# Performance work log

Measured on AMD Instinct MI355X. Metric: run time of the kernel, lower is better.

## Reference

```python
import jax, jax.numpy as jnp
import numpy as np

N, E, F_IN, HID, G = 20000, 320000, 128, 128, 64
H, D = 8, 32  # TransformerConv heads, per-head dim


def setup_inputs() -> dict:
    key = jax.random.key(0)
    ks = jax.random.split(key, 24)
    def w(k, i, o):
        return (jax.random.normal(k, (i, o), jnp.float32) / np.float32(np.sqrt(i)))
    def b(k, o):
        return jax.random.normal(k, (o,), jnp.float32) * 0.01
    inp = {
        'x': jax.random.normal(ks[0], (N, F_IN), jnp.float32),
        'edge_index': jax.random.randint(ks[1], (2, E), 0, N, jnp.int32),
        'batch': jnp.sort(jax.random.randint(ks[2], (N,), 0, G, jnp.int32)),
        # SAGEConv 1: 128 -> 128 (lin_l has bias, lin_r none)
        's1_wl': w(ks[3], 128, 128), 's1_bl': b(ks[4], 128), 's1_wr': w(ks[5], 128, 128),
        # SAGEConv 2: 128 -> 256
        's2_wl': w(ks[6], 128, 256), 's2_bl': b(ks[7], 256), 's2_wr': w(ks[8], 128, 256),
        # TransformerConv 1: 256 -> 8*32
        't1_wq': w(ks[9], 256, 256), 't1_bq': b(ks[10], 256),
        't1_wk': w(ks[11], 256, 256), 't1_bk': b(ks[12], 256),
        't1_wv': w(ks[13], 256, 256), 't1_bv': b(ks[14], 256),
        't1_ws': w(ks[15], 256, 256), 't1_bs': b(ks[16], 256),
        # TransformerConv 2
        't2_wq': w(ks[17], 256, 256), 't2_bq': b(ks[18], 256),
        't2_wk': w(ks[19], 256, 256), 't2_bk': b(ks[20], 256),
        't2_wv': w(ks[21], 256, 256), 't2_bv': b(ks[22], 256),
        't2_ws': w(ks[23], 256, 256), 't2_bs': b(jax.random.fold_in(key, 100), 256),
        # proj MLP: 256 -> 512 -> HID
        'p1_w': w(jax.random.fold_in(key, 101), 256, 512), 'p1_b': b(jax.random.fold_in(key, 102), 512),
        'p2_w': w(jax.random.fold_in(key, 103), 512, HID), 'p2_b': b(jax.random.fold_in(key, 104), HID),
    }
    return inp


def _sage(x, src, dst, wl, bl, wr):
    # PyG SAGEConv (aggr='mean'): lin_l(mean_j x_j) + lin_r(x_i)
    s = jax.ops.segment_sum(x[src], dst, num_segments=N)           # [N,F]
    cnt = jax.ops.segment_sum(jnp.ones((src.shape[0], 1), x.dtype), dst, num_segments=N)
    mean = s / jnp.maximum(cnt, 1.0)
    return mean @ wl + bl + x @ wr


def _tconv(x, src, dst, wq, bq, wk, bk, wv, bv, ws, bs):
    # PyG TransformerConv(256, 32, heads=8): per-edge attention + skip
    q = (x @ wq + bq).reshape(N, H, D)
    k = (x @ wk + bk).reshape(N, H, D)
    v = (x @ wv + bv).reshape(N, H, D)
    logits = jnp.einsum('ehd,ehd->eh', q[dst], k[src]) / np.float32(np.sqrt(D))  # [E,H]
    m = jax.ops.segment_max(logits, dst, num_segments=N)           # [N,H]
    p = jnp.exp(logits - m[dst])
    denom = jax.ops.segment_sum(p, dst, num_segments=N)
    p = p / denom[dst]                                              # softmax per target node per head
    agg = jax.ops.segment_sum(p[:, :, None] * v[src], dst, num_segments=N)  # [N,H,D]
    return agg.reshape(N, H * D) + x @ ws + bs


def reference(x, edge_index, batch, s1_wl, s1_bl, s1_wr, s2_wl, s2_bl, s2_wr,
              t1_wq, t1_bq, t1_wk, t1_bk, t1_wv, t1_bv, t1_ws, t1_bs,
              t2_wq, t2_bq, t2_wk, t2_bk, t2_wv, t2_bv, t2_ws, t2_bs,
              p1_w, p1_b, p2_w, p2_b):
    src, dst = edge_index[0], edge_index[1]
    h = jax.nn.relu(_sage(x, src, dst, s1_wl, s1_bl, s1_wr))
    h = jax.nn.relu(_sage(h, src, dst, s2_wl, s2_bl, s2_wr))
    h = jax.nn.relu(_tconv(h, src, dst, t1_wq, t1_bq, t1_wk, t1_bk, t1_wv, t1_bv, t1_ws, t1_bs))
    h = jax.nn.relu(_tconv(h, src, dst, t2_wq, t2_bq, t2_wk, t2_bk, t2_wv, t2_bv, t2_ws, t2_bs))
    # proj: ReLU -> Linear(256,512) -> ReLU -> Linear(512,HID) -> Sigmoid
    h = jax.nn.relu(h)
    h = jax.nn.relu(h @ p1_w + p1_b)
    h = jax.nn.sigmoid(h @ p2_w + p2_b)
    return jax.ops.segment_max(h, batch, num_segments=G)            # global_max_pool [G,HID]
```

## Files before the change

### kernel.cpp

```cpp
#include <hip/hip_runtime.h>
#include <hip/hip_bf16.h>
#include <math.h>

#define NN 20000
#define EE 320000
#define GG 64
#define CH 16

typedef __hip_bfloat16 bf16;
typedef __attribute__((ext_vector_type(8))) short short8;
typedef __attribute__((ext_vector_type(4))) float f32x4;
typedef unsigned int uint;
typedef unsigned short ushort;

__device__ __forceinline__ float bfr2f(ushort u) {
    union { uint i; float f; } c; c.i = ((uint)u) << 16; return c.f;
}
__device__ __forceinline__ ushort f2bfr(float f) {
    bf16 h = __float2bfloat16(f);
    return *(ushort*)&h;
}

__device__ __forceinline__ void load_lds16(const void* g, void* l) {
    __builtin_amdgcn_global_load_lds(
        (const __attribute__((address_space(1))) unsigned int*)g,
        (__attribute__((address_space(3))) unsigned int*)l, 16, 0, 0);
}

template <int KW, int NW, int KTOT, int KOFF>
__device__ __forceinline__ void tpose(int local, const float* __restrict__ W,
                                      bf16* __restrict__ Wt) {
    constexpr int SH = (KW == 128) ? 7 : ((KW == 256) ? 8 : 9);
    int n = local >> SH;
    int k = local & (KW - 1);
    Wt[(size_t)n * KTOT + KOFF + k] = __float2bfloat16(W[(size_t)k * NW + n]);
}

#define PREP_CONV  10000
#define PREP_PACK  (PREP_CONV + 3200)
#define PREP_BIAS  (PREP_PACK + 8)
#define PREP_COUNT (PREP_BIAS + 1250)

__global__ __launch_bounds__(256) void prep_kernel(
    const float* x, bf16* xm1,
    const float* s1_wr, const float* s1_wl, const float* s2_wr, const float* s2_wl,
    const float* t1_wq, const float* t1_wk, const float* t1_wv, const float* t1_ws,
    const float* t2_wq, const float* t2_wk, const float* t2_wv, const float* t2_ws,
    const float* p1_w, const float* p2_w,
    bf16* w1cat, bf16* w2cat, bf16* qw1, bf16* qw2, bf16* p1t, bf16* p2t,
    const float* b1q, const float* b1k, const float* b1v, const float* b1s,
    const float* b2q, const float* b2k, const float* b2v, const float* b2s,
    float* qb1, float* qb2,
    const int* dst, int* cnt) {
    int bid = blockIdx.x;
    int tid = threadIdx.x;
    if (bid < PREP_CONV) {
        int i = bid * 256 + tid;
        int r = i >> 7, c = i & 127;
        xm1[(size_t)r * 256 + c] = __float2bfloat16(x[i]);
    } else if (bid < PREP_PACK) {
        int i = (bid - PREP_CONV) * 256 + tid;
        if (i < 16384)        tpose<128, 128, 256, 0>(i, s1_wr, w1cat);
        else if (i < 32768)   tpose<128, 128, 256, 128>(i - 16384, s1_wl, w1cat);
        else if (i < 65536)   tpose<128, 256, 256, 0>(i - 32768, s2_wr, w2cat);
        else if (i < 98304)   tpose<128, 256, 256, 128>(i - 65536, s2_wl, w2cat);
        else if (i < 163840)  tpose<256, 256, 256, 0>(i - 98304,  t1_wq, qw1);
        else if (i < 229376)  tpose<256, 256, 256, 0>(i - 163840, t1_wk, qw1 + 65536);
        else if (i < 294912)  tpose<256, 256, 256, 0>(i - 229376, t1_wv, qw1 + 131072);
        else if (i < 360448)  tpose<256, 256, 256, 0>(i - 294912, t1_ws, qw1 + 196608);
        else if (i < 425984)  tpose<256, 256, 256, 0>(i - 360448, t2_wq, qw2);
        else if (i < 491520)  tpose<256, 256, 256, 0>(i - 425984, t2_wk, qw2 + 65536);
        else if (i < 557056)  tpose<256, 256, 256, 0>(i - 491520, t2_wv, qw2 + 131072);
        else if (i < 622592)  tpose<256, 256, 256, 0>(i - 557056, t2_ws, qw2 + 196608);
        else if (i < 753664)  tpose<256, 512, 256, 0>(i - 622592, p1_w, p1t);
        else if (i < 819200)  tpose<512, 128, 512, 0>(i - 753664, p2_w, p2t);
    } else if (bid < PREP_BIAS) {
        int i = (bid - PREP_PACK) * 256 + tid;
        if (i < 2048) {
            float* d = (i < 1024) ? qb1 : qb2;
            int j = i & 1023;
            const float* s;
            if (i < 1024) s = (j < 256) ? b1q : (j < 512) ? b1k : (j < 768) ? b1v : b1s;
            else          s = (j < 256) ? b2q : (j < 512) ? b2k : (j < 768) ? b2v : b2s;
            d[j] = s[j & 255];
        }
    } else {
        int e = (bid - PREP_BIAS) * 256 + tid;
        if (e < EE) atomicAdd(&cnt[dst[e]], 1);
    }
}

__global__ __launch_bounds__(1024) void scan_kernel(int* __restrict__ cnt,
                                                    int* __restrict__ off, int n) {
    __shared__ int wsum[16];
    __shared__ int carry_s;
    int tid = threadIdx.x;
    int lane = tid & 63, wid = tid >> 6;
    if (tid == 0) { carry_s = 0; off[0] = 0; }
    __syncthreads();
    for (int base = 0; base < n; base += 1024) {
        int idx = base + tid;
        int val = (idx < n) ? cnt[idx] : 0;
        int x = val;
        #pragma unroll
        for (int s = 1; s < 64; s <<= 1) {
            int y = __shfl_up(x, s, 64);
            if (lane >= s) x += y;
        }
        if (lane == 63) wsum[wid] = x;
        __syncthreads();
        if (tid == 0) {
            int c = carry_s;
            #pragma unroll
            for (int w = 0; w < 16; w++) { int t = wsum[w]; wsum[w] = c; c += t; }
            carry_s = c;
        }
        __syncthreads();
        int incl = wsum[wid] + x;
        if (idx < n) {
            off[idx + 1] = incl;
            cnt[idx] = incl - val;
        }
        __syncthreads();
    }
}

__global__ __launch_bounds__(256) void fill_kernel(const int* __restrict__ src,
                                                   const int* __restrict__ dst,
                                                   int* __restrict__ cursor,
                                                   int* __restrict__ csr_src, int E) {
    int e = blockIdx.x * 256 + threadIdx.x;
    if (e < E) {
        int p = atomicAdd(&cursor[dst[e]], 1);
        csr_src[p] = src[e];
    }
}

__global__ __launch_bounds__(256) void mean2_kernel(const bf16* __restrict__ x, int xstride,
                                                    const int* __restrict__ off,
                                                    const int* __restrict__ csr_src,
                                                    bf16* __restrict__ outp, int ostride) {
    int node = blockIdx.x * 4 + (threadIdx.x >> 6);
    int lane = threadIdx.x & 63;
    int e0 = off[node], e1 = off[node + 1];
    float s0 = 0.f, s1 = 0.f;
    int e = e0;
    for (; e + 7 < e1; e += 8) {
        uint a[8];
        #pragma unroll
        for (int j = 0; j < 8; j++) {
            int sa = csr_src[e + j];
            a[j] = *(const uint*)(x + (size_t)sa * xstride + lane * 2);
        }
        #pragma unroll
        for (int j = 0; j < 8; j++) {
            union { uint i; float f; } t;
            t.i = a[j] << 16; s0 += t.f;
            t.i = a[j] & 0xffff0000u; s1 += t.f;
        }
    }
    for (; e < e1; e++) {
        int sa = csr_src[e];
        uint a = *(const uint*)(x + (size_t)sa * xstride + lane * 2);
        union { uint i; float f; } t;
        t.i = a << 16; s0 += t.f; t.i = a & 0xffff0000u; s1 += t.f;
    }
    int deg = e1 - e0;
    float inv = (deg > 0) ? 1.f / (float)deg : 0.f;
    uint r = ((uint)f2bfr(s1 * inv) << 16) | (uint)f2bfr(s0 * inv);
    *(uint*)(outp + (size_t)node * ostride + lane * 2) = r;
}

template <int MODE, int TM>
__global__ __launch_bounds__(256, (TM == 128) ? 3 : 4)
void gemm_kernel(const bf16* __restrict__ A,
                 const bf16* __restrict__ Wt,
                 const float* __restrict__ bias,
                 void* __restrict__ Cv,
                 int M, int K, int N, int cstride,
                 const int* __restrict__ batch,
                 float* __restrict__ pool_out) {
    constexpr int NT = (TM == 128) ? 4 : 2;
    __shared__ short As[TM * 64];
    __shared__ short Bs[128 * 64];
    int t = threadIdx.x;
    int lane = t & 63;
    int wave = t >> 6;
    int wm = (TM == 128) ? (wave >> 1) * 64 : 0;
    int wn = (TM == 128) ? (wave & 1) * 64 : wave * 32;
    int bm = blockIdx.y * TM, bn = blockIdx.x * 128;
    int quad = lane >> 4, l16 = lane & 15;
    int srow = t >> 3;
    int scol = (t & 7) * 8;

    f32x4 acc[4][NT];
    f32x4 zero = {0.f, 0.f, 0.f, 0.f};
    #pragma unroll
    for (int i = 0; i < 4; i++)
        #pragma unroll
        for (int j = 0; j < NT; j++) acc[i][j] = zero;

    for (int kk = 0; kk < K; kk += 64) {
        #pragma unroll
        for (int r = 0; r < TM / 32; r++) {
            int row = r * 32 + srow;
            int gm = bm + row; gm = (gm < M) ? gm : (M - 1);
            load_lds16(A + (size_t)gm * K + kk + scol, &As[row * 64 + scol]);
        }
        #pragma unroll
        for (int r = 0; r < 4; r++) {
            int row = r * 32 + srow;
            load_lds16(Wt + (size_t)(bn + row) * K + kk + scol, &Bs[row * 64 + scol]);
        }
        __syncthreads();
        #pragma unroll
        for (int ks = 0; ks < 2; ks++) {
            short8 af[4], bfr[NT];
            #pragma unroll
            for (int i = 0; i < 4; i++)
                af[i] = *(const short8*)&As[(wm + i * 16 + l16) * 64 + ks * 32 + quad * 8];
            #pragma unroll
            for (int j = 0; j < NT; j++)
                bfr[j] = *(const short8*)&Bs[(wn + j * 16 + l16) * 64 + ks * 32 + quad * 8];
            #pragma unroll
            for (int i = 0; i < 4; i++)
                #pragma unroll
                for (int j = 0; j < NT; j++)
                    acc[i][j] = __builtin_amdgcn_mfma_f32_16x16x32_bf16(af[i], bfr[j], acc[i][j], 0, 0, 0);
        }
        __syncthreads();
    }

    #pragma unroll
    for (int i = 0; i < 4; i++) {
        int gm0 = bm + wm + i * 16 + quad * 4;
        #pragma unroll
        for (int j = 0; j < NT; j++) {
            int gn = bn + wn + j * 16 + l16;
            #pragma unroll
            for (int r = 0; r < 4; r++) {
                int gm = gm0 + r;
                if (gm >= M) continue;
                float v = acc[i][j][r] + bias[gn];
                if (MODE == 2) v = fmaxf(v, 0.f);
                if (MODE == 4) {
                    v = 1.f / (1.f + expf(-v));
                    atomicMax((int*)&pool_out[batch[gm] * 128 + gn], __float_as_int(v));
                } else {
                    ((bf16*)Cv)[(size_t)gm * cstride + gn] = __float2bfloat16(v);
                }
            }
        }
    }
}

template <int MODE, int TM>
static void launch_gemm(const bf16* A, const bf16* Wt, const float* bias, void* C,
                        int M, int K, int N, int cstride, hipStream_t st,
                        const int* batch = nullptr, float* pool_out = nullptr) {
    dim3 grid(N / 128, (M + TM - 1) / TM);
    hipLaunchKernelGGL((gemm_kernel<MODE, TM>), grid, dim3(256), 0, st,
                       A, Wt, bias, C, M, K, N, cstride, batch, pool_out);
}

__global__ __launch_bounds__(256) void attn4_kernel(const bf16* __restrict__ qkvs,
                                                    const int* __restrict__ off,
                                                    const int* __restrict__ csr_src,
                                                    bf16* __restrict__ out, int ostride) {
    __shared__ float pp[2][CH][9];
    __shared__ int srcs[2][CH];
    int i = blockIdx.x;
    int tid = threadIdx.x;
    int ea = tid >> 4, ha = (tid >> 1) & 7, half = tid & 1;
    int hc = tid >> 5;

    float qf[16];
    {
        const short8* qp = (const short8*)(qkvs + (size_t)i * 1024 + ha * 32 + half * 16);
        #pragma unroll
        for (int c = 0; c < 2; c++) {
            short8 v = qp[c];
            #pragma unroll
            for (int j = 0; j < 8; j++) qf[c * 8 + j] = bfr2f((ushort)v[j]);
        }
    }

    int e0 = off[i], e1 = off[i + 1];
    float l = 0.f, acc = 0.f;
    if (e0 < e1) {
        if (tid < CH) srcs[0][tid] = csr_src[min(e0 + tid, e1 - 1)];
        __syncthreads();
        int buf = 0;
        for (int base = e0; base < e1; base += CH, buf ^= 1) {
            int cnt = min(CH, e1 - base);
            ushort vv[CH];
            #pragma unroll
            for (int j = 0; j < CH; j++)
                vv[j] = *(const ushort*)(qkvs + (size_t)srcs[buf][j] * 1024 + 512 + tid);
            int s = srcs[buf][ea];
            const short8* kp = (const short8*)(qkvs + (size_t)s * 1024 + 256 + ha * 32 + half * 16);
            short8 k0 = kp[0];
            short8 k1 = kp[1];
            if (tid < CH) srcs[buf ^ 1][tid] = csr_src[min(base + CH + tid, e1 - 1)];
            float d = 0.f;
            #pragma unroll
            for (int j = 0; j < 8; j++) d += qf[j] * bfr2f((ushort)k0[j]);
            #pragma unroll
            for (int j = 0; j < 8; j++) d += qf[8 + j] * bfr2f((ushort)k1[j]);
            d += __shfl_xor(d, 1);
            float p = (ea < cnt) ? __expf(d * 0.17677669529663687f) : 0.f;
            if (half == 0) pp[buf][ea][ha] = p;
            __syncthreads();
            #pragma unroll
            for (int j = 0; j < CH; j++) {
                float pj = pp[buf][j][hc];
                l += pj;
                acc += pj * bfr2f(vv[j]);
            }
        }
    }
    float res = (l > 0.f) ? acc / l : 0.f;
    float val = res + bfr2f(*(const ushort*)(qkvs + (size_t)i * 1024 + 768 + tid));
    out[(size_t)i * ostride + tid] = __float2bfloat16(fmaxf(val, 0.f));
}

extern "C" void kernel_launch(void* const* d_in, const int* in_sizes, int n_in,
                              void* d_out, int out_size, void* d_ws, size_t ws_size,
                              hipStream_t stream) {
    const float* x      = (const float*)d_in[0];
    const int*   ei     = (const int*)d_in[1];
    const int*   batch  = (const int*)d_in[2];
    const float* s1_wl  = (const float*)d_in[3];
    const float* s1_bl  = (const float*)d_in[4];
    const float* s1_wr  = (const float*)d_in[5];
    const float* s2_wl  = (const float*)d_in[6];
    const float* s2_bl  = (const float*)d_in[7];
    const float* s2_wr  = (const float*)d_in[8];
    const float* t1_wq  = (const float*)d_in[9];
    const float* t1_bq  = (const float*)d_in[10];
    const float* t1_wk  = (const float*)d_in[11];
    const float* t1_bk  = (const float*)d_in[12];
    const float* t1_wv  = (const float*)d_in[13];
    const float* t1_bv  = (const float*)d_in[14];
    const float* t1_ws  = (const float*)d_in[15];
    const float* t1_bs  = (const float*)d_in[16];
    const float* t2_wq  = (const float*)d_in[17];
    const float* t2_bq  = (const float*)d_in[18];
    const float* t2_wk  = (const float*)d_in[19];
    const float* t2_bk  = (const float*)d_in[20];
    const float* t2_wv  = (const float*)d_in[21];
    const float* t2_bv  = (const float*)d_in[22];
    const float* t2_wsk = (const float*)d_in[23];
    const float* t2_bs  = (const float*)d_in[24];
    const float* p1_w   = (const float*)d_in[25];
    const float* p1_b   = (const float*)d_in[26];
    const float* p2_w   = (const float*)d_in[27];
    const float* p2_b   = (const float*)d_in[28];
    float* out = (float*)d_out;

    char* ws = (char*)d_ws;
    size_t o = 0;
    auto alloc = [&](size_t bytes) { char* p = ws + o; o += (bytes + 255) & ~(size_t)255; return p; };
    int* off     = (int*)alloc(sizeof(int) * (NN + 1));
    int* cursor  = (int*)alloc(sizeof(int) * NN);
    int* csr_src = (int*)alloc(sizeof(int) * EE);
    bf16* w1cat = (bf16*)alloc(2 * 128 * 256);
    bf16* w2cat = (bf16*)alloc(2 * 256 * 256);
    bf16* qw1   = (bf16*)alloc(2 * 1024 * 256);
    bf16* qw2   = (bf16*)alloc(2 * 1024 * 256);
    bf16* p1t   = (bf16*)alloc(2 * 512 * 256);
    bf16* p2t   = (bf16*)alloc(2 * 128 * 512);
    float* qb1  = (float*)alloc(4 * 1024);
    float* qb2  = (float*)alloc(4 * 1024);
    bf16* xm1   = (bf16*)alloc(2 * (size_t)NN * 256);
    bf16* xm2   = (bf16*)alloc(2 * (size_t)NN * 256);
    bf16* t1b   = (bf16*)alloc(2 * (size_t)NN * 512);
    bf16* Q     = (bf16*)alloc(2 * (size_t)NN * 1024);
    bf16* h2   = xm1;
    bf16* t1   = t1b;
    bf16* h4   = xm1;
    bf16* p1o  = t1b;

    const int* src = ei;
    const int* dst = ei + EE;

    hipMemsetAsync(cursor, 0, sizeof(int) * NN, stream);
    hipMemsetAsync(out, 0, sizeof(float) * (size_t)out_size, stream);

    prep_kernel<<<PREP_COUNT, 256, 0, stream>>>(
        x, xm1,
        s1_wr, s1_wl, s2_wr, s2_wl,
        t1_wq, t1_wk, t1_wv, t1_ws,
        t2_wq, t2_wk, t2_wv, t2_wsk,
        p1_w, p2_w,
        w1cat, w2cat, qw1, qw2, p1t, p2t,
        t1_bq, t1_bk, t1_bv, t1_bs,
        t2_bq, t2_bk, t2_bv, t2_bs,
        qb1, qb2,
        dst, cursor);

    scan_kernel<<<1, 1024, 0, stream>>>(cursor, off, NN);
    fill_kernel<<<(EE + 255) / 256, 256, 0, stream>>>(src, dst, cursor, csr_src, EE);

    mean2_kernel<<<NN / 4, 256, 0, stream>>>(xm1, 256, off, csr_src, xm1 + 128, 256);
    launch_gemm<2, 64>(xm1, w1cat, s1_bl, xm2, NN, 256, 128, 256, stream);

    mean2_kernel<<<NN / 4, 256, 0, stream>>>(xm2, 256, off, csr_src, xm2 + 128, 256);
    launch_gemm<2, 64>(xm2, w2cat, s2_bl, h2, NN, 256, 256, 256, stream);

    launch_gemm<0, 128>(h2, qw1, qb1, Q, NN, 256, 1024, 1024, stream);
    attn4_kernel<<<NN, 256, 0, stream>>>(Q, off, csr_src, t1, 256);

    launch_gemm<0, 128>(t1, qw2, qb2, Q, NN, 256, 1024, 1024, stream);
    attn4_kernel<<<NN, 256, 0, stream>>>(Q, off, csr_src, h4, 256);

    launch_gemm<2, 128>(h4, p1t, p1_b, p1o, NN, 256, 512, 512, stream);
    launch_gemm<4, 64>(p1o, p2t, p2_b, nullptr, NN, 512, 128, 128, stream, batch, out);
}
```

Baseline: 453.5 us.

## Store Q/K as fp16 for dot2 attention, vectorize V gather, pre-reduce pool max

The QKV GEMM epilogue now writes the Q and K columns as fp16, so the attention kernel can compute q·k with packed fp16 dot2 instructions instead of unpacking bf16 to float element by element. The V gather is widened so each thread loads two bf16 values per edge over half the edges, and partial sums are combined with a lane shuffle. The final GEMM's sigmoid+max-pool epilogue caches batch ids in LDS and reduces the per-graph max across the wave before issuing atomics, which cuts the atomic count. The cost is lower fp16 range and precision for the attention logits.

```diff
diff --git a/kernel.cpp b/kernel.cpp
--- a/kernel.cpp
+++ b/kernel.cpp
@@ -1,5 +1,6 @@
 #include <hip/hip_runtime.h>
 #include <hip/hip_bf16.h>
+#include <hip/hip_fp16.h>
 #include <math.h>
 
 #define NN 20000
@@ -10,6 +11,8 @@
 typedef __hip_bfloat16 bf16;
 typedef __attribute__((ext_vector_type(8))) short short8;
 typedef __attribute__((ext_vector_type(4))) float f32x4;
+typedef __attribute__((ext_vector_type(4))) uint uint4v;
+typedef __attribute__((ext_vector_type(2))) _Float16 half2v;
 typedef unsigned int uint;
 typedef unsigned short ushort;
 
@@ -19,6 +22,17 @@
 __device__ __forceinline__ ushort f2bfr(float f) {
     bf16 h = __float2bfloat16(f);
     return *(ushort*)&h;
+}
+
+__device__ __forceinline__ float dot2acc(uint a, uint b, float c) {
+#if __has_builtin(__builtin_amdgcn_fdot2)
+    return __builtin_amdgcn_fdot2(__builtin_bit_cast(half2v, a),
+                                  __builtin_bit_cast(half2v, b), c, false);
+#else
+    half2v ha = __builtin_bit_cast(half2v, a);
+    half2v hb = __builtin_bit_cast(half2v, b);
+    return c + (float)ha.x * (float)hb.x + (float)ha.y * (float)hb.y;
+#endif
 }
 
 __device__ __forceinline__ void load_lds16(const void* g, void* l) {
@@ -183,6 +197,7 @@
     constexpr int NT = (TM == 128) ? 4 : 2;
     __shared__ short As[TM * 64];
     __shared__ short Bs[128 * 64];
+    __shared__ int bat[TM];
     int t = threadIdx.x;
     int lane = t & 63;
     int wave = t >> 6;
@@ -193,6 +208,8 @@
     int srow = t >> 3;
     int scol = (t & 7) * 8;
 
+    if (MODE == 4 && t < TM) bat[t] = batch[min(bm + t, M - 1)];
+
     f32x4 acc[4][NT];
     f32x4 zero = {0.f, 0.f, 0.f, 0.f};
     #pragma unroll
@@ -229,6 +246,40 @@
                     acc[i][j] = __builtin_amdgcn_mfma_f32_16x16x32_bf16(af[i], bfr[j], acc[i][j], 0, 0, 0);
         }
         __syncthreads();
+    }
+
+    if (MODE == 4) {
+        int g0 = bat[0], gL = bat[TM - 1];
+        #pragma unroll
+        for (int j = 0; j < NT; j++) {
+            int gn = bn + wn + j * 16 + l16;
+            float m0 = 0.f, m1 = 0.f;
+            #pragma unroll
+            for (int i = 0; i < 4; i++) {
+                #pragma unroll
+                for (int r = 0; r < 4; r++) {
+                    int row = i * 16 + quad * 4 + r;
+                    int gm = bm + row;
+                    if (gm >= M) continue;
+                    float v = acc[i][j][r] + bias[gn];
+                    v = 1.f / (1.f + expf(-v));
+                    int g = bat[row];
+                    if (g == g0) m0 = fmaxf(m0, v);
+                    else if (g == gL) m1 = fmaxf(m1, v);
+                    else atomicMax((int*)&pool_out[g * 128 + gn], __float_as_int(v));
+                }
+            }
+            m0 = fmaxf(m0, __shfl_xor(m0, 16));
+            m0 = fmaxf(m0, __shfl_xor(m0, 32));
+            m1 = fmaxf(m1, __shfl_xor(m1, 16));
+            m1 = fmaxf(m1, __shfl_xor(m1, 32));
+            if (quad == 0) {
+                atomicMax((int*)&pool_out[g0 * 128 + gn], __float_as_int(m0));
+                if (gL != g0)
+                    atomicMax((int*)&pool_out[gL * 128 + gn], __float_as_int(m1));
+            }
+        }
+        return;
     }
 
     #pragma unroll
@@ -243,12 +294,14 @@
                 if (gm >= M) continue;
                 float v = acc[i][j][r] + bias[gn];
                 if (MODE == 2) v = fmaxf(v, 0.f);
-                if (MODE == 4) {
-                    v = 1.f / (1.f + expf(-v));
-                    atomicMax((int*)&pool_out[batch[gm] * 128 + gn], __float_as_int(v));
+                ushort st;
+                if (MODE == 5 && gn < 512) {
+                    __half hh = __float2half(v);
+                    st = *(ushort*)&hh;
                 } else {
-                    ((bf16*)Cv)[(size_t)gm * cstride + gn] = __float2bfloat16(v);
+                    st = f2bfr(v);
                 }
+                ((ushort*)Cv)[(size_t)gm * cstride + gn] = st;
             }
         }
     }
@@ -263,7 +316,7 @@
                        A, Wt, bias, C, M, K, N, cstride, batch, pool_out);
 }
 
-__global__ __launch_bounds__(256) void attn4_kernel(const bf16* __restrict__ qkvs,
+__global__ __launch_bounds__(256) void attn5_kernel(const bf16* __restrict__ qkvs,
                                                     const int* __restrict__ off,
                                                     const int* __restrict__ csr_src,
                                                     bf16* __restrict__ out, int ostride) {
@@ -272,56 +325,70 @@
     int i = blockIdx.x;
     int tid = threadIdx.x;
     int ea = tid >> 4, ha = (tid >> 1) & 7, half = tid & 1;
-    int hc = tid >> 5;
-
-    float qf[16];
+    int hc = tid >> 5, dp = (tid >> 1) & 15, epar = tid & 1;
+
+    uint q2[8];
     {
-        const short8* qp = (const short8*)(qkvs + (size_t)i * 1024 + ha * 32 + half * 16);
-        #pragma unroll
-        for (int c = 0; c < 2; c++) {
-            short8 v = qp[c];
-            #pragma unroll
-            for (int j = 0; j < 8; j++) qf[c * 8 + j] = bfr2f((ushort)v[j]);
-        }
+        const uint4v* qp = (const uint4v*)(qkvs + (size_t)i * 1024 + ha * 32 + half * 16);
+        uint4v a = qp[0], b = qp[1];
+        q2[0] = a.x; q2[1] = a.y; q2[2] = a.z; q2[3] = a.w;
+        q2[4] = b.x; q2[5] = b.y; q2[6] = b.z; q2[7] = b.w;
     }
 
     int e0 = off[i], e1 = off[i + 1];
-    float l = 0.f, acc = 0.f;
+    float l = 0.f, acc0 = 0.f, acc1 = 0.f;
+    int vcol = 512 + hc * 32 + dp * 2;
     if (e0 < e1) {
         if (tid < CH) srcs[0][tid] = csr_src[min(e0 + tid, e1 - 1)];
         __syncthreads();
         int buf = 0;
         for (int base = e0; base < e1; base += CH, buf ^= 1) {
             int cnt = min(CH, e1 - base);
-            ushort vv[CH];
-            #pragma unroll
-            for (int j = 0; j < CH; j++)
-                vv[j] = *(const ushort*)(qkvs + (size_t)srcs[buf][j] * 1024 + 512 + tid);
+            uint vv[8];
+            #pragma unroll
+            for (int j = 0; j < 8; j++) {
+                int e = epar + j * 2;
+                vv[j] = *(const uint*)(qkvs + (size_t)srcs[buf][e] * 1024 + vcol);
+            }
             int s = srcs[buf][ea];
-            const short8* kp = (const short8*)(qkvs + (size_t)s * 1024 + 256 + ha * 32 + half * 16);
-            short8 k0 = kp[0];
-            short8 k1 = kp[1];
+            const uint4v* kp = (const uint4v*)(qkvs + (size_t)s * 1024 + 256 + ha * 32 + half * 16);
+            uint4v ka = kp[0], kb = kp[1];
             if (tid < CH) srcs[buf ^ 1][tid] = csr_src[min(base + CH + tid, e1 - 1)];
             float d = 0.f;
-            #pragma unroll
-            for (int j = 0; j < 8; j++) d += qf[j] * bfr2f((ushort)k0[j]);
-            #pragma unroll
-            for (int j = 0; j < 8; j++) d += qf[8 + j] * bfr2f((ushort)k1[j]);
+            d = dot2acc(q2[0], ka.x, d); d = dot2acc(q2[1], ka.y, d);
+            d = dot2acc(q2[2], ka.z, d); d = dot2acc(q2[3], ka.w, d);
+            d = dot2acc(q2[4], kb.x, d); d = dot2acc(q2[5], kb.y, d);
+            d = dot2acc(q2[6], kb.z, d); d = dot2acc(q2[7], kb.w, d);
             d += __shfl_xor(d, 1);
             float p = (ea < cnt) ? __expf(d * 0.17677669529663687f) : 0.f;
             if (half == 0) pp[buf][ea][ha] = p;
             __syncthreads();
             #pragma unroll
-            for (int j = 0; j < CH; j++) {
-                float pj = pp[buf][j][hc];
+            for (int j = 0; j < 8; j++) {
+                int e = epar + j * 2;
+                float pj = pp[buf][e][hc];
                 l += pj;
-                acc += pj * bfr2f(vv[j]);
+                union { uint i; float f; } lo, hi;
+                lo.i = vv[j] << 16; hi.i = vv[j] & 0xffff0000u;
+                acc0 += pj * lo.f;
+                acc1 += pj * hi.f;
             }
         }
     }
-    float res = (l > 0.f) ? acc / l : 0.f;
-    float val = res + bfr2f(*(const ushort*)(qkvs + (size_t)i * 1024 + 768 + tid));
-    out[(size_t)i * ostride + tid] = __float2bfloat16(fmaxf(val, 0.f));
+    acc0 += __shfl_xor(acc0, 1);
+    acc1 += __shfl_xor(acc1, 1);
+    l    += __shfl_xor(l, 1);
+    float inv = (l > 0.f) ? 1.f / l : 0.f;
+    float r0 = acc0 * inv, r1 = acc1 * inv;
+    if (epar == 0) {
+        uint su = *(const uint*)(qkvs + (size_t)i * 1024 + 768 + hc * 32 + dp * 2);
+        union { uint i; float f; } lo, hi;
+        lo.i = su << 16; hi.i = su & 0xffff0000u;
+        float v0 = fmaxf(r0 + lo.f, 0.f);
+        float v1 = fmaxf(r1 + hi.f, 0.f);
+        uint packed = ((uint)f2bfr(v1) << 16) | (uint)f2bfr(v0);
+        *(uint*)(out + (size_t)i * ostride + hc * 32 + dp * 2) = packed;
+    }
 }
 
 extern "C" void kernel_launch(void* const* d_in, const int* in_sizes, int n_in,
@@ -408,11 +475,11 @@
     mean2_kernel<<<NN / 4, 256, 0, stream>>>(xm2, 256, off, csr_src, xm2 + 128, 256);
     launch_gemm<2, 64>(xm2, w2cat, s2_bl, h2, NN, 256, 256, 256, stream);
 
-    launch_gemm<0, 128>(h2, qw1, qb1, Q, NN, 256, 1024, 1024, stream);
-    attn4_kernel<<<NN, 256, 0, stream>>>(Q, off, csr_src, t1, 256);
-
-    launch_gemm<0, 128>(t1, qw2, qb2, Q, NN, 256, 1024, 1024, stream);
-    attn4_kernel<<<NN, 256, 0, stream>>>(Q, off, csr_src, h4, 256);
+    launch_gemm<5, 128>(h2, qw1, qb1, Q, NN, 256, 1024, 1024, stream);
+    attn5_kernel<<<NN, 256, 0, stream>>>(Q, off, csr_src, t1, 256);
+
+    launch_gemm<5, 128>(t1, qw2, qb2, Q, NN, 256, 1024, 1024, stream);
+    attn5_kernel<<<NN, 256, 0, stream>>>(Q, off, csr_src, h4, 256);
 
     launch_gemm<2, 128>(h4, p1t, p1_b, p1o, NN, 256, 512, 512, stream);
     launch_gemm<4, 64>(p1o, p2t, p2_b, nullptr, NN, 512, 128, 128, stream, batch, out);
```

New measurement: 437.5 us. 1.04x faster.
